# Kernel tuning notes

Hardware: AMD Instinct MI355X
Metric: run time of the kernel (lower is better)

Reference implementation:

```python
import jax, jax.numpy as jnp
import numpy as np

POS_MARGIN = 0.01
NEG_MARGIN = 0.2
REG_WEIGHT = 0.1
N, D = 8192, 256
NUM_CLASSES = 512


def setup_inputs() -> dict:
    key = jax.random.key(0)
    k1, k2 = jax.random.split(key)
    embeds = jax.random.normal(k1, (N, D), dtype=jnp.float32)
    labels = jax.random.randint(k2, (N,), 0, NUM_CLASSES, dtype=jnp.int64)
    return {"embeds": embeds, "labels": labels}


def reference(embeds, labels):
    n, d = embeds.shape
    # L2-normalize embeddings (normalize_embeds=True)
    e = embeds / jnp.linalg.norm(embeds, axis=1, keepdims=True)

    # var(e_i - e_j, ddof=1) over feature dim, computed without the [N,N,D] tensor:
    # var = (D/(D-1)) * ( mean(e_i^2) + mean(e_j^2) - 2*mean(e_i*e_j) - (m_i - m_j)^2 )
    m = e.mean(axis=1)                      # [N]
    s = (e * e).mean(axis=1)                # [N]
    g = (e @ e.T) / d                       # [N,N] = mean(e_i * e_j) over D
    corr = d / (d - 1.0)
    var_diff = corr * (s[:, None] + s[None, :] - 2.0 * g - (m[:, None] - m[None, :]) ** 2)
    row_var = corr * (s - m * m)            # torch.var(e, dim=1), unbiased
    distmat = var_diff / row_var[:, None]

    same = labels[:, None] == labels[None, :]
    eye = jnp.eye(n, dtype=bool)
    pos_mask = same & (~eye)                # all same-label pairs (anchor != positive)
    neg_mask = ~same                        # all diff-label pairs

    pos_l = jax.nn.relu(distmat - POS_MARGIN) * pos_mask
    neg_l = jax.nn.relu(NEG_MARGIN - distmat) * neg_mask

    # avg_nonzero_only=True: sum / (# strictly-positive entries + 1e-12)
    pos_loss = pos_l.sum() / ((pos_l > 0).sum().astype(jnp.float32) + 1e-12)
    neg_loss = neg_l.sum() / ((neg_l > 0).sum().astype(jnp.float32) + 1e-12)

    loss = pos_loss + neg_loss
    loss = loss + jnp.abs(e.sum(axis=1)).mean() * REG_WEIGHT
    return loss
```

## Files before the change

### kernel.cpp

```cpp
#include <hip/hip_runtime.h>

#define NROWS 8192
#define DDIM 256
#define BT 128
#define BK 64
#define GT (NROWS / BT)
#define NBT (GT * (GT + 1) / 2)

using bf16x8 = __attribute__((ext_vector_type(8))) __bf16;
using f32x4  = __attribute__((ext_vector_type(4))) float;

__device__ __forceinline__ void glds16(const unsigned short* g, unsigned short* l) {
    __builtin_amdgcn_global_load_lds(
        (const __attribute__((address_space(1))) unsigned int*)g,
        (__attribute__((address_space(3))) unsigned int*)l,
        16, 0, 0);
}

__device__ __forceinline__ unsigned short f2bf(float f) {
    unsigned int b = __float_as_uint(f);
    unsigned int r = b + 0x7fffu + ((b >> 16) & 1u);
    return (unsigned short)(r >> 16);
}

__global__ __launch_bounds__(256) void rowstats_kernel(
    const float* __restrict__ x, unsigned short* __restrict__ ebf,
    float* __restrict__ aP, float* __restrict__ bs,
    float* __restrict__ rabs)
{
    int wave = threadIdx.x >> 6;
    int lane = threadIdx.x & 63;
    int row  = blockIdx.x * 4 + wave;

    const float4 v = reinterpret_cast<const float4*>(x + (size_t)row * DDIM)[lane];
    float ss = v.x * v.x + v.y * v.y + v.z * v.z + v.w * v.w;
    float sm = v.x + v.y + v.z + v.w;
    #pragma unroll
    for (int off = 32; off >= 1; off >>= 1) {
        ss += __shfl_xor(ss, off);
        sm += __shfl_xor(sm, off);
    }
    float invn = 1.0f / sqrtf(ss);
    float m = sm * invn * (1.0f / DDIM);

    ushort4 o;
    o.x = f2bf(v.x * invn - m);
    o.y = f2bf(v.y * invn - m);
    o.z = f2bf(v.z * invn - m);
    o.w = f2bf(v.w * invn - m);
    reinterpret_cast<ushort4*>(ebf + (size_t)row * DDIM)[lane] = o;

    if (lane == 0) {
        float s  = ss * invn * invn * (1.0f / DDIM);
        float b  = s - m * m;
        float a  = 1.0f / b;
        aP[row]   = a * (1.0f / 128.0f);
        bs[row]   = -128.0f * b;
        rabs[row] = fabsf(sm * invn);
    }
}

__global__ __launch_bounds__(256) void snr_gemm_kernel(
    const unsigned short* __restrict__ ebf,
    const float* __restrict__ aP, const float* __restrict__ bs,
    const int* __restrict__ labels,
    float* __restrict__ partials)
{
    __shared__ __align__(16) unsigned short As[BT * BK];
    __shared__ __align__(16) unsigned short Bs[BT * BK];
    __shared__ float sAPi[BT], sBsi[BT];
    __shared__ float sAPj[BT], sBsj[BT];
    __shared__ int   sLi[BT], sLj[BT];
    __shared__ float redbuf[4][4];

    int tid  = threadIdx.x;
    int lane = tid & 63;
    int wave = tid >> 6;
    int wr = (wave >> 1) * 64;
    int wc = (wave & 1) * 64;

    int t = blockIdx.x;
    int bi = (int)((2.0f * GT + 1.0f
                    - sqrtf((2.0f * GT + 1.0f) * (2.0f * GT + 1.0f) - 8.0f * (float)t)) * 0.5f);
    while ((bi + 1) * GT - ((bi + 1) * bi) / 2 <= t) ++bi;
    while (bi * GT - (bi * (bi - 1)) / 2 > t) --bi;
    int bj = bi + (t - (bi * GT - (bi * (bi - 1)) / 2));
    int rowBase = bi * BT, colBase = bj * BT;
    bool diag = (bi == bj);

    if (tid < BT) {
        int gi = rowBase + tid;
        sAPi[tid] = aP[gi]; sBsi[tid] = bs[gi];
        sLi[tid] = labels[gi];
    } else {
        int tt = tid - BT;
        int gj = colBase + tt;
        sAPj[tt] = aP[gj]; sBsj[tt] = bs[gj];
        sLj[tt] = labels[gj];
    }

    const unsigned short* gA[4];
    const unsigned short* gB[4];
    unsigned short* lpA[4];
    unsigned short* lpB[4];
    #pragma unroll
    for (int p = 0; p < 4; ++p) {
        int q   = p * 256 + tid;
        int row = q >> 3;
        int kc  = (q & 7) ^ (row & 7);
        gA[p] = ebf + (size_t)(rowBase + row) * DDIM + kc * 8;
        gB[p] = ebf + (size_t)(colBase + row) * DDIM + kc * 8;
        lpA[p] = As + q * 8;
        lpB[p] = Bs + q * 8;
    }

    int mrow = lane & 15;
    int kch  = lane >> 4;
    int offA[4][2], offB[4][2];
    #pragma unroll
    for (int t4 = 0; t4 < 4; ++t4) {
        int rA = wr + t4 * 16 + mrow;
        int rB = wc + t4 * 16 + mrow;
        #pragma unroll
        for (int h = 0; h < 2; ++h) {
            offA[t4][h] = (rA * 8 + ((h * 4 + kch) ^ (rA & 7))) * 8;
            offB[t4][h] = (rB * 8 + ((h * 4 + kch) ^ (rB & 7))) * 8;
        }
    }

    f32x4 acc[4][4];
    #pragma unroll
    for (int a = 0; a < 4; ++a)
        #pragma unroll
        for (int b = 0; b < 4; ++b)
            acc[a][b] = (f32x4){0.f, 0.f, 0.f, 0.f};

    for (int it = 0; it < 4; ++it) {
        #pragma unroll
        for (int p = 0; p < 4; ++p) {
            glds16(gA[p], lpA[p]);
            glds16(gB[p], lpB[p]);
            gA[p] += BK;
            gB[p] += BK;
        }
        asm volatile("s_waitcnt vmcnt(0)" ::: "memory");
        __syncthreads();

        #pragma unroll
        for (int h = 0; h < 2; ++h) {
            bf16x8 aF[4], bF[4];
            #pragma unroll
            for (int t4 = 0; t4 < 4; ++t4) {
                aF[t4] = *reinterpret_cast<const bf16x8*>(As + offA[t4][h]);
                bF[t4] = *reinterpret_cast<const bf16x8*>(Bs + offB[t4][h]);
            }
            #pragma unroll
            for (int ti = 0; ti < 4; ++ti)
                #pragma unroll
                for (int tj = 0; tj < 4; ++tj)
                    acc[ti][tj] = __builtin_amdgcn_mfma_f32_16x16x32_bf16(aF[ti], bF[tj], acc[ti][tj], 0, 0, 0);
        }
        __syncthreads();
    }

    int subr = (lane >> 4) * 4;
    int cj   = lane & 15;

    float aPC[4], bsC[4];
    int LCj[4];
    #pragma unroll
    for (int tj = 0; tj < 4; ++tj) {
        int lj = wc + tj * 16 + cj;
        aPC[tj] = sAPj[lj]; bsC[tj] = sBsj[lj];
        LCj[tj] = sLj[lj];
    }

    float Sn = 0.f, Sp = 0.f;
    unsigned Cn = 0u, Cp = 0u;

    if (!diag) {
        #pragma unroll
        for (int ti = 0; ti < 4; ++ti) {
            #pragma unroll
            for (int r = 0; r < 4; ++r) {
                int li = wr + ti * 16 + subr + r;
                float aR = sAPi[li], bR = sBsi[li];
                int LR = sLi[li];
                #pragma unroll
                for (int tj = 0; tj < 4; ++tj) {
                    float raw = acc[ti][tj][r];
                    float v1 = fmaf(aR, raw + bsC[tj], -0.8f);
                    float v2 = fmaf(aPC[tj], raw + bR, -0.8f);
                    bool same = (LR == LCj[tj]);
                    unsigned long long b1 = __ballot(v1 > 0.f);
                    unsigned long long b2 = __ballot(v2 > 0.f);
                    unsigned long long ms = __ballot(same);
                    if (b1 | b2 | ms) {
                        float nz = fmaxf(v1, 0.f) + fmaxf(v2, 0.f);
                        Sn += same ? 0.f : nz;
                        float pz = fmaxf(0.19f - v1, 0.f) + fmaxf(0.19f - v2, 0.f);
                        Sp += same ? pz : 0.f;
                        Cn += (unsigned)__popcll(b1 & ~ms)
                            + (unsigned)__popcll(b2 & ~ms);
                        Cp += (unsigned)__popcll(__ballot(v1 < 0.19f) & ms)
                            + (unsigned)__popcll(__ballot(v2 < 0.19f) & ms);
                    }
                }
            }
        }
    } else {
        #pragma unroll
        for (int ti = 0; ti < 4; ++ti) {
            #pragma unroll
            for (int r = 0; r < 4; ++r) {
                int li = wr + ti * 16 + subr + r;
                float aR = sAPi[li];
                int LR = sLi[li];
                #pragma unroll
                for (int tj = 0; tj < 4; ++tj) {
                    int lj = wc + tj * 16 + cj;
                    float raw = acc[ti][tj][r];
                    float v1 = fmaf(aR, raw + bsC[tj], -0.8f);
                    bool same = (LR == LCj[tj]);
                    bool pok  = same && (li != lj);
                    unsigned long long b1 = __ballot(v1 > 0.f);
                    unsigned long long ms = __ballot(same);
                    if (b1 | ms) {
                        unsigned long long mp = __ballot(pok);
                        Sn += same ? 0.f : fmaxf(v1, 0.f);
                        float pz = fmaxf(0.19f - v1, 0.f);
                        Sp += pok ? pz : 0.f;
                        Cn += (unsigned)__popcll(b1 & ~ms);
                        Cp += (unsigned)__popcll(__ballot(v1 < 0.19f) & mp);
                    }
                }
            }
        }
    }

    #pragma unroll
    for (int off = 32; off >= 1; off >>= 1) {
        Sn += __shfl_down(Sn, off);
        Sp += __shfl_down(Sp, off);
    }
    if (lane == 0) {
        redbuf[wave][0] = Sn; redbuf[wave][1] = (float)Cn;
        redbuf[wave][2] = Sp; redbuf[wave][3] = (float)Cp;
    }
    __syncthreads();
    if (tid < 4) {
        partials[blockIdx.x * 4 + tid] =
            redbuf[0][tid] + redbuf[1][tid] + redbuf[2][tid] + redbuf[3][tid];
    }
}

__global__ __launch_bounds__(256) void finalize_kernel(
    const float* __restrict__ partials, const float* __restrict__ rabs,
    float* __restrict__ out)
{
    int tid = threadIdx.x;
    float s0 = 0, s1 = 0, s2 = 0, s3 = 0, rr = 0;
    for (int i = tid; i < NBT; i += 256) {
        float4 p = reinterpret_cast<const float4*>(partials)[i];
        s0 += p.x; s1 += p.y; s2 += p.z; s3 += p.w;
    }
    for (int i = tid; i < NROWS; i += 256) rr += rabs[i];

    #pragma unroll
    for (int off = 32; off >= 1; off >>= 1) {
        s0 += __shfl_down(s0, off);
        s1 += __shfl_down(s1, off);
        s2 += __shfl_down(s2, off);
        s3 += __shfl_down(s3, off);
        rr += __shfl_down(rr, off);
    }
    __shared__ float red[4][5];
    int wave = tid >> 6, lane = tid & 63;
    if (lane == 0) {
        red[wave][0] = s0; red[wave][1] = s1; red[wave][2] = s2;
        red[wave][3] = s3; red[wave][4] = rr;
    }
    __syncthreads();
    if (tid == 0) {
        float a0 = 0, a1 = 0, a2 = 0, a3 = 0, a4 = 0;
        #pragma unroll
        for (int w = 0; w < 4; ++w) {
            a0 += red[w][0]; a1 += red[w][1]; a2 += red[w][2];
            a3 += red[w][3]; a4 += red[w][4];
        }
        float neg = (a1 > 0.5f) ? a0 / (a1 + 1e-12f) : 0.0f;
        float pos = (a3 > 0.5f) ? a2 / (a3 + 1e-12f) : 0.0f;
        out[0] = pos + neg + a4 * (0.1f / (float)NROWS);
    }
}

extern "C" void kernel_launch(void* const* d_in, const int* in_sizes, int n_in,
                              void* d_out, int out_size, void* d_ws, size_t ws_size,
                              hipStream_t stream) {
    const float* embeds = (const float*)d_in[0];
    const int*   labels = (const int*)d_in[1];
    float* out = (float*)d_out;

    char* ws = (char*)d_ws;
    unsigned short* ebf = (unsigned short*)ws;
    float* aP   = (float*)(ws + (size_t)NROWS * DDIM * 2);
    float* bs   = aP + NROWS;
    float* rabs = bs + NROWS;
    float* partials = rabs + NROWS;

    rowstats_kernel<<<NROWS / 4, 256, 0, stream>>>(embeds, ebf, aP, bs, rabs);

    snr_gemm_kernel<<<NBT, 256, 0, stream>>>(ebf, aP, bs, labels, partials);

    finalize_kernel<<<1, 256, 0, stream>>>(partials, rabs, out);
}
```

Before: 102.6 us.

## Double-buffer LDS tiles to overlap global loads with MFMA compute

After: 109.0 us. 6.3% more time.

```diff
diff --git a/kernel.cpp b/kernel.cpp
--- a/kernel.cpp
+++ b/kernel.cpp
@@ -66,8 +66,8 @@
     const int* __restrict__ labels,
     float* __restrict__ partials)
 {
-    __shared__ __align__(16) unsigned short As[BT * BK];
-    __shared__ __align__(16) unsigned short Bs[BT * BK];
+    __shared__ __align__(16) unsigned short As[2][BT * BK];
+    __shared__ __align__(16) unsigned short Bs[2][BT * BK];
     __shared__ float sAPi[BT], sBsi[BT];
     __shared__ float sAPj[BT], sBsj[BT];
     __shared__ int   sLi[BT], sLj[BT];
@@ -101,8 +101,7 @@
 
     const unsigned short* gA[4];
     const unsigned short* gB[4];
-    unsigned short* lpA[4];
-    unsigned short* lpB[4];
+    int qoff[4];
     #pragma unroll
     for (int p = 0; p < 4; ++p) {
         int q   = p * 256 + tid;
@@ -110,8 +109,7 @@
         int kc  = (q & 7) ^ (row & 7);
         gA[p] = ebf + (size_t)(rowBase + row) * DDIM + kc * 8;
         gB[p] = ebf + (size_t)(colBase + row) * DDIM + kc * 8;
-        lpA[p] = As + q * 8;
-        lpB[p] = Bs + q * 8;
+        qoff[p] = q * 8;
     }
 
     int mrow = lane & 15;
@@ -135,24 +133,39 @@
         for (int b = 0; b < 4; ++b)
             acc[a][b] = (f32x4){0.f, 0.f, 0.f, 0.f};
 
+    #pragma unroll
+    for (int p = 0; p < 4; ++p) {
+        glds16(gA[p], &As[0][qoff[p]]);
+        glds16(gB[p], &Bs[0][qoff[p]]);
+        gA[p] += BK;
+        gB[p] += BK;
+    }
+    asm volatile("s_waitcnt lgkmcnt(0)" ::: "memory");
+
+    #pragma unroll
     for (int it = 0; it < 4; ++it) {
-        #pragma unroll
-        for (int p = 0; p < 4; ++p) {
-            glds16(gA[p], lpA[p]);
-            glds16(gB[p], lpB[p]);
-            gA[p] += BK;
-            gB[p] += BK;
-        }
-        asm volatile("s_waitcnt vmcnt(0)" ::: "memory");
-        __syncthreads();
+        int cur = it & 1;
+        if (it < 3) {
+            #pragma unroll
+            for (int p = 0; p < 4; ++p) {
+                glds16(gA[p], &As[cur ^ 1][qoff[p]]);
+                glds16(gB[p], &Bs[cur ^ 1][qoff[p]]);
+                gA[p] += BK;
+                gB[p] += BK;
+            }
+            asm volatile("s_waitcnt vmcnt(8)" ::: "memory");
+        } else {
+            asm volatile("s_waitcnt vmcnt(0)" ::: "memory");
+        }
+        asm volatile("s_barrier" ::: "memory");
 
         #pragma unroll
         for (int h = 0; h < 2; ++h) {
             bf16x8 aF[4], bF[4];
             #pragma unroll
             for (int t4 = 0; t4 < 4; ++t4) {
-                aF[t4] = *reinterpret_cast<const bf16x8*>(As + offA[t4][h]);
-                bF[t4] = *reinterpret_cast<const bf16x8*>(Bs + offB[t4][h]);
+                aF[t4] = *reinterpret_cast<const bf16x8*>(&As[cur][0] + offA[t4][h]);
+                bF[t4] = *reinterpret_cast<const bf16x8*>(&Bs[cur][0] + offB[t4][h]);
             }
             #pragma unroll
             for (int ti = 0; ti < 4; ++ti)
@@ -160,7 +173,8 @@
                 for (int tj = 0; tj < 4; ++tj)
                     acc[ti][tj] = __builtin_amdgcn_mfma_f32_16x16x32_bf16(aF[ti], bF[tj], acc[ti][tj], 0, 0, 0);
         }
-        __syncthreads();
+        if (it < 3)
+            asm volatile("s_barrier" ::: "memory");
     }
 
     int subr = (lane >> 4) * 4;
```
